# Kernel tuning notes

Hardware: AMD Instinct MI355X
Metric: run time of the kernel (lower is better)

## Reference

```python
import jax, jax.numpy as jnp
import numpy as np


def setup_inputs() -> dict:
    key = jax.random.key(0)
    k1, k2, k3 = jax.random.split(key, 3)
    B, H, W = 4, 1024, 1024
    D, Hg, Wg = 8, 16, 16
    C = 12  # (Cin+1)*Cout = (3+1)*3
    grid = jax.random.normal(k1, (B, C, D, Hg, Wg), dtype=jnp.float32)
    guide = jax.random.uniform(k2, (B, H, W), dtype=jnp.float32)
    image = jax.random.normal(k3, (B, 3, H, W), dtype=jnp.float32)
    return {"grid": grid, "guide": guide, "image": image}


def _slice_coeffs(grid, guide):
    """Guide-indexed trilinear slice of the bilateral grid.

    grid:  [B, C, D, Hg, Wg]; guide: [B, H, W] in [0,1].
    Returns per-pixel coefficients [B, H, W, C].
    """
    B, C, D, Hg, Wg = grid.shape
    _, H, W = guide.shape
    grid_t = jnp.transpose(grid, (0, 2, 3, 4, 1))  # [B, D, Hg, Wg, C]

    # grid-space coordinates of each pixel (HDRNet convention)
    gx = (jnp.arange(W, dtype=grid.dtype) + 0.5) * Wg / W   # [W]
    gy = (jnp.arange(H, dtype=grid.dtype) + 0.5) * Hg / H   # [H]
    gz = guide * D                                          # [B, H, W]

    fx = jnp.floor(gx - 0.5)
    fy = jnp.floor(gy - 0.5)
    fz = jnp.floor(gz - 0.5)

    bb = jnp.arange(B)[:, None, None]
    coeff = jnp.zeros((B, H, W, C), dtype=grid.dtype)
    for dz in (0, 1):
        zz = fz + dz
        wz = jnp.maximum(1.0 - jnp.abs(zz + 0.5 - gz), 0.0)     # [B,H,W]
        zi = jnp.clip(zz, 0, D - 1).astype(jnp.int32)
        for dy in (0, 1):
            yy = fy + dy
            wy = jnp.maximum(1.0 - jnp.abs(yy + 0.5 - gy), 0.0)  # [H]
            yi = jnp.clip(yy, 0, Hg - 1).astype(jnp.int32)
            for dx in (0, 1):
                xx = fx + dx
                wx = jnp.maximum(1.0 - jnp.abs(xx + 0.5 - gx), 0.0)  # [W]
                xi = jnp.clip(xx, 0, Wg - 1).astype(jnp.int32)
                w = wz * wy[None, :, None] * wx[None, None, :]       # [B,H,W]
                c = grid_t[bb, zi, yi[None, :, None], xi[None, None, :]]  # [B,H,W,C]
                coeff = coeff + w[..., None] * c
    return coeff


def reference(grid, guide, image):
    B, Cin, H, W = image.shape
    coeff = _slice_coeffs(grid, guide)                 # [B,H,W,(Cin+1)*Cout]
    Cout = coeff.shape[-1] // (Cin + 1)
    coeff = coeff.reshape(B, H, W, Cout, Cin + 1)
    # per-pixel affine: out[c] = sum_j A[c,j] * image[j] + bias[c]
    out = jnp.einsum('bhwcj,bjhw->bchw', coeff[..., :Cin], image)
    out = out + jnp.transpose(coeff[..., Cin], (0, 3, 1, 2))
    return out
```

## Files before the change

### kernel.cpp

```cpp
#include <hip/hip_runtime.h>

#define BB 4
#define CC 12
#define DD 8
#define HG 16
#define WG 16
#define HH 1024
#define WW 1024

typedef float vf4 __attribute__((ext_vector_type(4)));

#define XSTRIDE 104
#define ROWS 4

__global__ __launch_bounds__(256) void slice_apply(
    const float* __restrict__ grid,
    const float* __restrict__ guide,
    const float* __restrict__ img,
    float* __restrict__ out)
{
    __shared__ float S[ROWS * WG * XSTRIDE];

    const int blk = blockIdx.x;
    const int b  = blk >> 8;
    const int h0 = (blk & 255) * ROWS;

    const float gy0 = (h0 + 0.5f) * ((float)HG / (float)HH);
    const float fy  = floorf(gy0 - 0.5f);
    const int   iy0 = max(0, min(HG - 1, (int)fy));
    const int   iy1 = max(0, min(HG - 1, (int)fy + 1));

    float wy1r[ROWS];
    #pragma unroll
    for (int r = 0; r < ROWS; ++r) {
        const float gy = (h0 + r + 0.5f) * ((float)HG / (float)HH);
        wy1r[r] = gy - 0.5f - fy;
    }

    for (int j = threadIdx.x; j < CC * DD * WG; j += 256) {
        const int x = j & 15;
        const int z = (j >> 4) & 7;
        const int c = j >> 7;
        const size_t base = ((size_t)(b * CC + c) * DD + z) * (HG * WG);
        const float v0 = grid[base + iy0 * WG + x];
        const float v1 = grid[base + iy1 * WG + x];
        const int so = x * XSTRIDE + z * CC + c;
        #pragma unroll
        for (int r = 0; r < ROWS; ++r) {
            const float ty = wy1r[r];
            S[r * (WG * XSTRIDE) + so] = v0 + ty * (v1 - v0);
        }
    }
    __syncthreads();

    const int w0 = threadIdx.x * 4;

    const float scale = (float)WG / (float)WW;
    const float gx0 = (w0 + 0.5f) * scale;
    const float fx  = floorf(gx0 - 0.5f);
    const float tx0 = gx0 - 0.5f - fx;
    const int   ix0 = max(0, min(WG - 1, (int)fx));
    const int   ix1 = max(0, min(WG - 1, (int)fx + 1));

    #pragma unroll
    for (int r = 0; r < ROWS; ++r) {
        const int h = h0 + r;
        const float* Sr  = S + r * (WG * XSTRIDE);
        const float* Sx0 = Sr + ix0 * XSTRIDE;
        const float* Sx1 = Sr + ix1 * XSTRIDE;

        const size_t pix = ((size_t)b * HH + h) * WW + w0;
        const vf4 g4 = *reinterpret_cast<const vf4*>(guide + pix);
        const float* ib = img + (((size_t)b * 3) * HH + h) * WW + w0;
        const vf4 i0 = __builtin_nontemporal_load(reinterpret_cast<const vf4*>(ib));
        const vf4 i1 = __builtin_nontemporal_load(reinterpret_cast<const vf4*>(ib + (size_t)HH * WW));
        const vf4 i2 = __builtin_nontemporal_load(reinterpret_cast<const vf4*>(ib + (size_t)2 * HH * WW));

        vf4 o0, o1, o2;

        #pragma unroll
        for (int p = 0; p < 4; ++p) {
            const float tx  = tx0 + (float)p * scale;
            const float wx0 = 1.0f - tx, wx1 = tx;

            const float gv = g4[p];
            const float gz  = gv * (float)DD;
            const float fz  = floorf(gz - 0.5f);
            const float tz  = gz - 0.5f - fz;
            const int   iz0 = max(0, min(DD - 1, (int)fz));
            const int   iz1 = max(0, min(DD - 1, (int)fz + 1));
            const float wz0 = 1.0f - tz, wz1 = tz;

            const float w00 = wz0 * wx0, w01 = wz0 * wx1;
            const float w10 = wz1 * wx0, w11 = wz1 * wx1;

            float acc[12];
            #pragma unroll
            for (int k = 0; k < 12; ++k) acc[k] = 0.0f;

            auto accum = [&](const float* P, float w) {
                const vf4 a = *reinterpret_cast<const vf4*>(P);
                const vf4 e = *reinterpret_cast<const vf4*>(P + 4);
                const vf4 f = *reinterpret_cast<const vf4*>(P + 8);
                #pragma unroll
                for (int k = 0; k < 4; ++k) {
                    acc[k]     += w * a[k];
                    acc[4 + k] += w * e[k];
                    acc[8 + k] += w * f[k];
                }
            };
            accum(Sx0 + iz0 * CC, w00);
            accum(Sx1 + iz0 * CC, w01);
            accum(Sx0 + iz1 * CC, w10);
            accum(Sx1 + iz1 * CC, w11);

            const float im0 = i0[p];
            const float im1 = i1[p];
            const float im2 = i2[p];

            o0[p] = acc[0] * im0 + acc[1] * im1 + acc[2]  * im2 + acc[3];
            o1[p] = acc[4] * im0 + acc[5] * im1 + acc[6]  * im2 + acc[7];
            o2[p] = acc[8] * im0 + acc[9] * im1 + acc[10] * im2 + acc[11];
        }

        float* ob = out + (((size_t)b * 3) * HH + h) * WW + w0;
        __builtin_nontemporal_store(o0, reinterpret_cast<vf4*>(ob));
        __builtin_nontemporal_store(o1, reinterpret_cast<vf4*>(ob + (size_t)HH * WW));
        __builtin_nontemporal_store(o2, reinterpret_cast<vf4*>(ob + (size_t)2 * HH * WW));
    }
}

extern "C" void kernel_launch(void* const* d_in, const int* in_sizes, int n_in,
                              void* d_out, int out_size, void* d_ws, size_t ws_size,
                              hipStream_t stream) {
    const float* grid  = (const float*)d_in[0];
    const float* guide = (const float*)d_in[1];
    const float* image = (const float*)d_in[2];
    float* out = (float*)d_out;

    const int nblocks = BB * HH / ROWS;
    slice_apply<<<nblocks, 256, 0, stream>>>(grid, guide, image, out);
}
```

Measured before the change: 121.5 us.

## Prefetch pixel inputs before grid staging and halve rows per block

The per-row guide and image loads are issued at kernel start, before the shared-memory grid staging and barrier, so global-memory latency overlaps the slice setup. Rows per block drop from 4 to 2, doubling the block count and halving shared memory per block. The shared x-stride shrinks from 104 to 100 and the accumulators become vector types. In exchange, more registers hold prefetched data, and grid staging work is repeated across twice as many blocks.

```diff
diff --git a/kernel.cpp b/kernel.cpp
--- a/kernel.cpp
+++ b/kernel.cpp
@@ -10,8 +10,8 @@
 
 typedef float vf4 __attribute__((ext_vector_type(4)));
 
-#define XSTRIDE 104
-#define ROWS 4
+#define XSTRIDE 100
+#define ROWS 2
 
 __global__ __launch_bounds__(256) void slice_apply(
     const float* __restrict__ grid,
@@ -22,19 +22,32 @@
     __shared__ float S[ROWS * WG * XSTRIDE];
 
     const int blk = blockIdx.x;
-    const int b  = blk >> 8;
-    const int h0 = (blk & 255) * ROWS;
+    const int b  = blk >> 9;
+    const int h0 = (blk & 511) * ROWS;
 
     const float gy0 = (h0 + 0.5f) * ((float)HG / (float)HH);
     const float fy  = floorf(gy0 - 0.5f);
     const int   iy0 = max(0, min(HG - 1, (int)fy));
     const int   iy1 = max(0, min(HG - 1, (int)fy + 1));
 
-    float wy1r[ROWS];
+    float tyr[ROWS];
     #pragma unroll
     for (int r = 0; r < ROWS; ++r) {
         const float gy = (h0 + r + 0.5f) * ((float)HG / (float)HH);
-        wy1r[r] = gy - 0.5f - fy;
+        tyr[r] = gy - 0.5f - fy;
+    }
+
+    const int w0 = threadIdx.x * 4;
+    vf4 g4v[ROWS], i0v[ROWS], i1v[ROWS], i2v[ROWS];
+    #pragma unroll
+    for (int r = 0; r < ROWS; ++r) {
+        const int h = h0 + r;
+        const size_t pix = ((size_t)b * HH + h) * WW + w0;
+        g4v[r] = *reinterpret_cast<const vf4*>(guide + pix);
+        const float* ib = img + (((size_t)b * 3) * HH + h) * WW + w0;
+        i0v[r] = __builtin_nontemporal_load(reinterpret_cast<const vf4*>(ib));
+        i1v[r] = __builtin_nontemporal_load(reinterpret_cast<const vf4*>(ib + (size_t)HH * WW));
+        i2v[r] = __builtin_nontemporal_load(reinterpret_cast<const vf4*>(ib + (size_t)2 * HH * WW));
     }
 
     for (int j = threadIdx.x; j < CC * DD * WG; j += 256) {
@@ -46,14 +59,10 @@
         const float v1 = grid[base + iy1 * WG + x];
         const int so = x * XSTRIDE + z * CC + c;
         #pragma unroll
-        for (int r = 0; r < ROWS; ++r) {
-            const float ty = wy1r[r];
-            S[r * (WG * XSTRIDE) + so] = v0 + ty * (v1 - v0);
-        }
+        for (int r = 0; r < ROWS; ++r)
+            S[r * (WG * XSTRIDE) + so] = v0 + tyr[r] * (v1 - v0);
     }
     __syncthreads();
-
-    const int w0 = threadIdx.x * 4;
 
     const float scale = (float)WG / (float)WW;
     const float gx0 = (w0 + 0.5f) * scale;
@@ -69,13 +78,8 @@
         const float* Sx0 = Sr + ix0 * XSTRIDE;
         const float* Sx1 = Sr + ix1 * XSTRIDE;
 
-        const size_t pix = ((size_t)b * HH + h) * WW + w0;
-        const vf4 g4 = *reinterpret_cast<const vf4*>(guide + pix);
-        const float* ib = img + (((size_t)b * 3) * HH + h) * WW + w0;
-        const vf4 i0 = __builtin_nontemporal_load(reinterpret_cast<const vf4*>(ib));
-        const vf4 i1 = __builtin_nontemporal_load(reinterpret_cast<const vf4*>(ib + (size_t)HH * WW));
-        const vf4 i2 = __builtin_nontemporal_load(reinterpret_cast<const vf4*>(ib + (size_t)2 * HH * WW));
-
+        const vf4 g4 = g4v[r];
+        const vf4 i0 = i0v[r], i1 = i1v[r], i2 = i2v[r];
         vf4 o0, o1, o2;
 
         #pragma unroll
@@ -83,8 +87,7 @@
             const float tx  = tx0 + (float)p * scale;
             const float wx0 = 1.0f - tx, wx1 = tx;
 
-            const float gv = g4[p];
-            const float gz  = gv * (float)DD;
+            const float gz  = g4[p] * (float)DD;
             const float fz  = floorf(gz - 0.5f);
             const float tz  = gz - 0.5f - fz;
             const int   iz0 = max(0, min(DD - 1, (int)fz));
@@ -94,20 +97,15 @@
             const float w00 = wz0 * wx0, w01 = wz0 * wx1;
             const float w10 = wz1 * wx0, w11 = wz1 * wx1;
 
-            float acc[12];
-            #pragma unroll
-            for (int k = 0; k < 12; ++k) acc[k] = 0.0f;
+            vf4 accA = 0.0f, accB = 0.0f, accC = 0.0f;
 
             auto accum = [&](const float* P, float w) {
                 const vf4 a = *reinterpret_cast<const vf4*>(P);
                 const vf4 e = *reinterpret_cast<const vf4*>(P + 4);
                 const vf4 f = *reinterpret_cast<const vf4*>(P + 8);
-                #pragma unroll
-                for (int k = 0; k < 4; ++k) {
-                    acc[k]     += w * a[k];
-                    acc[4 + k] += w * e[k];
-                    acc[8 + k] += w * f[k];
-                }
+                accA += w * a;
+                accB += w * e;
+                accC += w * f;
             };
             accum(Sx0 + iz0 * CC, w00);
             accum(Sx1 + iz0 * CC, w01);
@@ -118,9 +116,9 @@
             const float im1 = i1[p];
             const float im2 = i2[p];
 
-            o0[p] = acc[0] * im0 + acc[1] * im1 + acc[2]  * im2 + acc[3];
-            o1[p] = acc[4] * im0 + acc[5] * im1 + acc[6]  * im2 + acc[7];
-            o2[p] = acc[8] * im0 + acc[9] * im1 + acc[10] * im2 + acc[11];
+            o0[p] = accA[0] * im0 + accA[1] * im1 + accA[2] * im2 + accA[3];
+            o1[p] = accB[0] * im0 + accB[1] * im1 + accB[2] * im2 + accB[3];
+            o2[p] = accC[0] * im0 + accC[1] * im1 + accC[2] * im2 + accC[3];
         }
 
         float* ob = out + (((size_t)b * 3) * HH + h) * WW + w0;
```

New measurement: 123.8 us. No clear change (+1.9%).
